# Kernel tuning notes

Hardware: AMD Instinct MI355X
Metric: run time of the kernel (lower is better)

Reference implementation:

```python
import jax, jax.numpy as jnp
import numpy as np

B, D, T, R = 8, 128, 32768, 2
C = D // R  # reduced channel dim = 64


def conv1x1(x, w, b):
    # x: [B, Cin, T], w: [Cout, Cin], b: [Cout] -> [B, Cout, T]
    return jnp.einsum('oi,bit->bot', w, x) + b[None, :, None]


def setup_inputs() -> dict:
    key = jax.random.key(0)
    ks = jax.random.split(key, 16)
    inp = {
        'x1': jax.random.normal(ks[0], (B, D, T), dtype=jnp.float32),
        'x2': jnp.zeros((B, D, T), dtype=jnp.float32),  # unused in encoder stage
        'mask': jnp.ones((B, 1, T), dtype=jnp.float32),
        # 1x1 conv projections (weights squeezed to [out, in])
        'wq': jax.random.normal(ks[1], (C, D), dtype=jnp.float32) * 0.05,
        'bq': jnp.zeros((C,), dtype=jnp.float32),
        'wk': jax.random.normal(ks[2], (C, D), dtype=jnp.float32) * 0.05,
        'bk': jnp.zeros((C,), dtype=jnp.float32),
        'wv': jax.random.normal(ks[3], (C, D), dtype=jnp.float32) * 0.05,
        'bv': jnp.zeros((C,), dtype=jnp.float32),
        # E, F: Linear(C -> C) with bias
        'we': jax.random.normal(ks[4], (C, C), dtype=jnp.float32) * 0.1,
        'be': jnp.zeros((C,), dtype=jnp.float32),
        'wf': jax.random.normal(ks[5], (C, C), dtype=jnp.float32) * 0.1,
        'bf': jnp.zeros((C,), dtype=jnp.float32),
        # output 1x1 conv: C -> D
        'wo': jax.random.normal(ks[6], (D, C), dtype=jnp.float32) * 0.05,
        'bo': jnp.zeros((D,), dtype=jnp.float32),
    }
    return inp


def reference(x1, x2, mask, wq, bq, wk, bk, wv, bv, we, be, wf, bf, wo, bo):
    # Q/K/V projections (encoder stage: value from x1; x2 unused)
    Q = conv1x1(x1, wq, bq)              # [B, C, T]
    K = conv1x1(x1, wk, bk)              # [B, C, T]
    V = conv1x1(x1, wv, bv)              # [B, C, T]
    # K = E(K^T): [B, T, C] @ we^T + be
    Kp = jnp.einsum('bct,oc->bto', K, we) + be  # [B, T, C]
    # S = Q @ Kp -> [B, C, C], scaled by sqrt(last dim)
    S = jnp.einsum('bct,btk->bck', Q, Kp)
    P = jax.nn.softmax(S / jnp.sqrt(jnp.asarray(S.shape[-1], S.dtype)), axis=-1)
    # dropout is identity in eval mode
    # V = (F(V^T))^T: [B, C, T]
    Vp = jnp.einsum('bct,oc->bot', V, wf) + bf[None, :, None]  # [B, C, T]
    out = jnp.einsum('bck,bkt->bct', P, Vp)  # [B, C, T]
    out = conv1x1(jax.nn.relu(out), wo, bo)  # [B, D, T]
    return out * mask[:, 0:1, :]
```

## Files before the change

### kernel.cpp

```cpp
#include <hip/hip_runtime.h>
#include <stdint.h>
#include <stddef.h>

#define B_ 8
#define D_ 128
#define T_ 32768
#define C_ 64
#define NCH_ 64

typedef __bf16 bf16;
typedef __bf16 bf16x4 __attribute__((ext_vector_type(4)));
typedef __bf16 bf16x8 __attribute__((ext_vector_type(8)));
typedef float f32x2 __attribute__((ext_vector_type(2)));
typedef float f32x4 __attribute__((ext_vector_type(4)));
typedef float f32x16 __attribute__((ext_vector_type(16)));

__device__ __forceinline__ f32x16 zero16() {
  f32x16 z;
#pragma unroll
  for (int i = 0; i < 16; ++i) z[i] = 0.f;
  return z;
}

__global__ __launch_bounds__(256) void k0_zero(float* __restrict__ p, int n)
{
  int i = blockIdx.x * 256 + threadIdx.x;
  if (i < n) p[i] = 0.f;
}

__global__ __launch_bounds__(256, 2) void k1_gram(
    const float* __restrict__ x1,
    const float* __restrict__ we, const float* __restrict__ wk,
    const float* __restrict__ bk, const float* __restrict__ be,
    const float* __restrict__ wf, const float* __restrict__ wv,
    const float* __restrict__ bv, const float* __restrict__ bfv,
    const float* __restrict__ wo,
    float* __restrict__ G, float* __restrict__ r,
    float* __restrict__ wkp, float* __restrict__ wvp,
    float* __restrict__ bkp, float* __restrict__ bvp,
    bf16* __restrict__ wobf,
    float* __restrict__ gpart)
{
  const int blk = blockIdx.x;
  const int tid = threadIdx.x;
  const int ngram = B_ * NCH_;

  if (blk >= ngram) {
    const int wb = blk - ngram;
    if (wb < 64) {
      const float* wa  = (wb < 32) ? we : wf;
      const float* wb2 = (wb < 32) ? wk : wv;
      float* outw      = (wb < 32) ? wkp : wvp;
      const int idx = (wb & 31) * 256 + tid;
      const int o = idx >> 7, d = idx & 127;
      float s = 0.f;
      for (int c = 0; c < 64; ++c) s += wa[o * 64 + c] * wb2[c * 128 + d];
      outw[idx] = s;
      if (tid < 64) {
        if (wb == 0) {
          float t = 0.f;
          for (int c = 0; c < 64; ++c) t += we[tid * 64 + c] * bk[c];
          bkp[tid] = t + be[tid];
        } else if (wb == 32) {
          float t = 0.f;
          for (int c = 0; c < 64; ++c) t += wf[tid * 64 + c] * bv[c];
          bvp[tid] = t + bfv[tid];
        }
      }
    } else {
      const int idx = (wb - 64) * 256 + tid;
      wobf[idx] = (bf16)wo[idx];
    }
    return;
  }

  __shared__ bf16 x_s[128 * 264];

  const int b  = blk / NCH_;
  const int ch = blk & (NCH_ - 1);
  const int t0 = ch * (T_ / NCH_);
  const int wave = tid >> 6, lane = tid & 63;
  const int lrow = lane & 31, lk = lane >> 5;
  const int qa = wave >> 1, qb = wave & 1;

  const float* xb = x1 + (size_t)b * D_ * T_ + t0;

  f32x16 acc00 = zero16(), acc01 = zero16(), acc10 = zero16(), acc11 = zero16();
  float rsum = 0.f;

  const bf16* A0  = &x_s[(64 * qa + lrow) * 264 + 8 * lk];
  const bf16* A1  = A0 + 32 * 264;
  const bf16* Bb0 = &x_s[(64 * qb + lrow) * 264 + 8 * lk];
  const bf16* Bb1 = Bb0 + 32 * 264;

  for (int s = 0; s < 2; ++s) {
    const float* xs = xb + s * 256;
    if (s) __syncthreads();
#pragma unroll
    for (int g = 0; g < 4; ++g) {
      f32x4 pre[8];
#pragma unroll
      for (int i = 0; i < 8; ++i) {
        const int row = 32 * wave + 8 * g + i;
        pre[i] = *(const f32x4*)(xs + (size_t)row * T_ + 4 * lane);
      }
#pragma unroll
      for (int i = 0; i < 8; ++i) {
        const int row = 32 * wave + 8 * g + i;
        bf16x4 h;
#pragma unroll
        for (int j = 0; j < 4; ++j) h[j] = (bf16)pre[i][j];
        *(bf16x4*)&x_s[row * 264 + 4 * lane] = h;
      }
    }
    __syncthreads();
#pragma unroll
    for (int k = 0; k < 16; ++k) {
      bf16x8 fa0 = *(const bf16x8*)(A0 + 16 * k);
      bf16x8 fa1 = *(const bf16x8*)(A1 + 16 * k);
      bf16x8 fb0 = *(const bf16x8*)(Bb0 + 16 * k);
      bf16x8 fb1 = *(const bf16x8*)(Bb1 + 16 * k);
      bf16x8 own = qb ? fa1 : fa0;
#pragma unroll
      for (int j = 0; j < 8; ++j) rsum += (float)own[j];
      acc00 = __builtin_amdgcn_mfma_f32_32x32x16_bf16(fa0, fb0, acc00, 0, 0, 0);
      acc01 = __builtin_amdgcn_mfma_f32_32x32x16_bf16(fa0, fb1, acc01, 0, 0, 0);
      acc10 = __builtin_amdgcn_mfma_f32_32x32x16_bf16(fa1, fb0, acc10, 0, 0, 0);
      acc11 = __builtin_amdgcn_mfma_f32_32x32x16_bf16(fa1, fb1, acc11, 0, 0, 0);
    }
  }

  if (gpart) {
    float* gp = gpart + (size_t)blk * 16384 + wave * 4096;
#pragma unroll
    for (int rr = 0; rr < 16; ++rr) {
      f32x4 v;
      v[0] = acc00[rr]; v[1] = acc01[rr]; v[2] = acc10[rr]; v[3] = acc11[rr];
      *(f32x4*)(gp + rr * 256 + lane * 4) = v;
    }
  } else {
    float* gb = G + (size_t)b * 16384;
#pragma unroll
    for (int rr = 0; rr < 16; ++rr) {
      const int rloc = (rr & 3) + 8 * (rr >> 2) + 4 * lk;
      const int r0 = 64 * qa + rloc, r1 = 64 * qa + 32 + rloc;
      const int c0 = 64 * qb + lrow, c1 = 64 * qb + 32 + lrow;
      atomicAdd(&gb[r0 * 128 + c0], acc00[rr]);
      atomicAdd(&gb[r0 * 128 + c1], acc01[rr]);
      atomicAdd(&gb[r1 * 128 + c0], acc10[rr]);
      atomicAdd(&gb[r1 * 128 + c1], acc11[rr]);
    }
  }
  float rtot = rsum + __shfl_xor(rsum, 32, 64);
  if (lk == 0) atomicAdd(&r[b * 128 + 32 * wave + lrow], rtot);
}

__global__ __launch_bounds__(256) void k2_reduce(
    const float* __restrict__ gpart, float* __restrict__ G)
{
  const int g4 = blockIdx.x * 256 + threadIdx.x;
  const int b = g4 >> 12;
  const int e4 = g4 & 4095;
  const f32x4* p = (const f32x4*)(gpart + ((size_t)b * NCH_) * 16384) + e4;
  f32x4 s = {0.f, 0.f, 0.f, 0.f};
#pragma unroll 8
  for (int ch = 0; ch < NCH_; ++ch) s += p[(size_t)ch * 4096];

  const int w = e4 >> 10, rr = (e4 >> 6) & 15, lane = e4 & 63;
  const int lk = lane >> 5, lrow = lane & 31;
  const int qa = w >> 1, qb = w & 1;
  const int rloc = (rr & 3) + 8 * (rr >> 2) + 4 * lk;
  const int r0 = 64 * qa + rloc, c0 = 64 * qb + lrow;
  float* Gb = G + (size_t)b * 16384;
  Gb[r0 * 128 + c0]               = s[0];
  Gb[r0 * 128 + c0 + 32]          = s[1];
  Gb[(r0 + 32) * 128 + c0]        = s[2];
  Gb[(r0 + 32) * 128 + c0 + 32]   = s[3];
}

__global__ __launch_bounds__(128) void k3_softmax(
    const float* __restrict__ wq, const float* __restrict__ bq,
    const float* __restrict__ G, const float* __restrict__ r,
    const float* __restrict__ wkp, const float* __restrict__ wvp,
    const float* __restrict__ bkp, const float* __restrict__ bvp,
    bf16* __restrict__ attw, float* __restrict__ attb)
{
  const int b = blockIdx.x >> 6, c = blockIdx.x & 63;
  const int tid = threadIdx.x;
  __shared__ float sM[128], sR[128], sQ[128], sP[64];
  __shared__ float sRed;

  const float* Gb = G + (size_t)b * 16384;
  const float* wqc = wq + c * 128;

  const float rv = r[b * 128 + tid];
  sR[tid] = rv;
  float m = 0.f;
  for (int j = 0; j < 128; ++j) m += wqc[j] * Gb[j * 128 + tid];
  sM[tid] = m;
  sQ[tid] = wqc[tid] * rv;
  __syncthreads();

  if (tid < 64) {
    float q2 = sQ[tid] + sQ[tid + 64];
#pragma unroll
    for (int off = 32; off; off >>= 1) q2 += __shfl_xor(q2, off, 64);
    if (tid == 0) sRed = q2;
  }
  __syncthreads();
  const float qr = sRed;
  const float bqc = bq[c];

  if (tid < 64) {
    const int k = tid;
    float s = 0.f, wkr = 0.f;
    for (int i = 0; i < 128; ++i) {
      const float w = wkp[k * 128 + i];
      s += sM[i] * w;
      wkr += sR[i] * w;
    }
    const float bk2 = bkp[k];
    float logit = (s + bqc * wkr + bk2 * qr + (float)T_ * bqc * bk2) * 0.125f;
    float mx = logit;
#pragma unroll
    for (int off = 32; off; off >>= 1) mx = fmaxf(mx, __shfl_xor(mx, off, 64));
    const float e = __expf(logit - mx);
    float sum = e;
#pragma unroll
    for (int off = 32; off; off >>= 1) sum += __shfl_xor(sum, off, 64);
    sP[k] = e / sum;
  }
  __syncthreads();

  {
    float aw = 0.f;
    for (int k = 0; k < 64; ++k) aw += sP[k] * wvp[k * 128 + tid];
    attw[((size_t)b * 64 + c) * 128 + tid] = (bf16)aw;
  }
  if (tid < 64) {
    float pb = sP[tid] * bvp[tid];
#pragma unroll
    for (int off = 32; off; off >>= 1) pb += __shfl_xor(pb, off, 64);
    if (tid == 0) attb[b * 64 + c] = pb;
  }
}

__global__ __launch_bounds__(256, 4) void k4_out(
    const float* __restrict__ x1, const float* __restrict__ mask,
    const bf16* __restrict__ wobf, const float* __restrict__ bo,
    const bf16* __restrict__ attw, const float* __restrict__ attb,
    float* __restrict__ out)
{
  __shared__ __attribute__((aligned(16))) char ubuf[64 * 132 * 4];
  bf16*  m1  = (bf16*)ubuf;
  float* o_s = (float*)ubuf;
  __shared__ float bo_s[128];
  __shared__ float ab_s[64];

  const int b = blockIdx.x >> 8;
  const int t0 = (blockIdx.x & 255) << 7;
  const int tid = threadIdx.x;
  const int wave = tid >> 6, lane = tid & 63;
  const int lrow = lane & 31, lk = lane >> 5;
  const int tcol = 32 * wave + lrow;

  if (tid < 128) bo_s[tid] = bo[tid];
  if (tid < 64) ab_s[tid] = attb[b * 64 + tid];
  __syncthreads();

  const float* xc = x1 + (size_t)b * D_ * T_ + t0 + tcol;
  const bf16* awb = attw + (size_t)b * 8192;

  f32x16 p0 = zero16(), p1 = zero16();
#pragma unroll
  for (int k0 = 0; k0 < 8; ++k0) {
    bf16x8 a0 = *(const bf16x8*)(awb + (size_t)lrow * 128 + 16 * k0 + 8 * lk);
    bf16x8 a1 = *(const bf16x8*)(awb + (size_t)(32 + lrow) * 128 + 16 * k0 + 8 * lk);
    bf16x8 bx;
#pragma unroll
    for (int j = 0; j < 8; ++j)
      bx[j] = (bf16)xc[(size_t)(16 * k0 + 8 * lk + j) * T_];
    p0 = __builtin_amdgcn_mfma_f32_32x32x16_bf16(a0, bx, p0, 0, 0, 0);
    p1 = __builtin_amdgcn_mfma_f32_32x32x16_bf16(a1, bx, p1, 0, 0, 0);
  }
  bf16* mrow = &m1[tcol * 72];
#pragma unroll
  for (int rr = 0; rr < 16; ++rr) {
    const int row = (rr & 3) + 8 * (rr >> 2) + 4 * lk;
    mrow[row]      = (bf16)fmaxf(p0[rr] + ab_s[row], 0.f);
    mrow[32 + row] = (bf16)fmaxf(p1[rr] + ab_s[32 + row], 0.f);
  }

  f32x16 q0 = zero16(), q1 = zero16(), q2 = zero16(), q3 = zero16();
#pragma unroll
  for (int k0 = 0; k0 < 4; ++k0) {
    bf16x8 bm = *(const bf16x8*)(mrow + 16 * k0 + 8 * lk);
    bf16x8 w0 = *(const bf16x8*)(wobf + (size_t)(lrow) * 64 + 16 * k0 + 8 * lk);
    bf16x8 w1 = *(const bf16x8*)(wobf + (size_t)(32 + lrow) * 64 + 16 * k0 + 8 * lk);
    bf16x8 w2 = *(const bf16x8*)(wobf + (size_t)(64 + lrow) * 64 + 16 * k0 + 8 * lk);
    bf16x8 w3 = *(const bf16x8*)(wobf + (size_t)(96 + lrow) * 64 + 16 * k0 + 8 * lk);
    q0 = __builtin_amdgcn_mfma_f32_32x32x16_bf16(w0, bm, q0, 0, 0, 0);
    q1 = __builtin_amdgcn_mfma_f32_32x32x16_bf16(w1, bm, q1, 0, 0, 0);
    q2 = __builtin_amdgcn_mfma_f32_32x32x16_bf16(w2, bm, q2, 0, 0, 0);
    q3 = __builtin_amdgcn_mfma_f32_32x32x16_bf16(w3, bm, q3, 0, 0, 0);
  }

  const float mv = mask[(size_t)b * T_ + t0 + tcol];
  float* ob = out + (size_t)b * D_ * T_ + t0;

  __syncthreads();
#pragma unroll
  for (int rr = 0; rr < 16; ++rr) {
    const int rloc = (rr & 3) + 8 * (rr >> 2) + 4 * lk;
    o_s[rloc * 132 + tcol]        = (q0[rr] + bo_s[rloc]) * mv;
    o_s[(32 + rloc) * 132 + tcol] = (q1[rr] + bo_s[32 + rloc]) * mv;
  }
  __syncthreads();
#pragma unroll
  for (int i = 0; i < 16; ++i) {
    const int dl = 16 * wave + i;
    f32x2 v = *(const f32x2*)(o_s + dl * 132 + 2 * lane);
    *(f32x2*)(ob + (size_t)dl * T_ + 2 * lane) = v;
  }
  __syncthreads();
#pragma unroll
  for (int rr = 0; rr < 16; ++rr) {
    const int rloc = (rr & 3) + 8 * (rr >> 2) + 4 * lk;
    o_s[rloc * 132 + tcol]        = (q2[rr] + bo_s[64 + rloc]) * mv;
    o_s[(32 + rloc) * 132 + tcol] = (q3[rr] + bo_s[96 + rloc]) * mv;
  }
  __syncthreads();
#pragma unroll
  for (int i = 0; i < 16; ++i) {
    const int dl = 16 * wave + i;
    f32x2 v = *(const f32x2*)(o_s + dl * 132 + 2 * lane);
    *(f32x2*)(ob + (size_t)(64 + dl) * T_ + 2 * lane) = v;
  }
}

extern "C" void kernel_launch(void* const* d_in, const int* in_sizes, int n_in,
                              void* d_out, int out_size, void* d_ws, size_t ws_size,
                              hipStream_t stream)
{
  const float* x1   = (const float*)d_in[0];
  const float* mask = (const float*)d_in[2];
  const float* wq   = (const float*)d_in[3];
  const float* bq   = (const float*)d_in[4];
  const float* wk   = (const float*)d_in[5];
  const float* bk   = (const float*)d_in[6];
  const float* wv   = (const float*)d_in[7];
  const float* bv   = (const float*)d_in[8];
  const float* we   = (const float*)d_in[9];
  const float* be   = (const float*)d_in[10];
  const float* wf   = (const float*)d_in[11];
  const float* bfv  = (const float*)d_in[12];
  const float* wo   = (const float*)d_in[13];
  const float* bo   = (const float*)d_in[14];
  float* out = (float*)d_out;

  char* base = (char*)d_ws;
  size_t off = 0;
  float* G    = (float*)(base + off); off += (size_t)B_ * 16384 * 4;
  float* r    = (float*)(base + off); off += (size_t)B_ * 128 * 4;
  float* wkp  = (float*)(base + off); off += 8192 * 4;
  float* wvp  = (float*)(base + off); off += 8192 * 4;
  float* bkp  = (float*)(base + off); off += 64 * 4;
  float* bvp  = (float*)(base + off); off += 64 * 4;
  float* attb = (float*)(base + off); off += (size_t)B_ * 64 * 4;
  bf16* attw  = (bf16*)(base + off);  off += (size_t)B_ * 64 * 128 * 2;
  bf16* wobf  = (bf16*)(base + off);  off += 8192 * 2;
  off = (off + 15) & ~(size_t)15;
  float* gpart = (float*)(base + off);
  const size_t need = off + (size_t)B_ * NCH_ * 16384 * 4;
  const bool use_part = (ws_size >= need);
  if (!use_part) gpart = nullptr;

  if (use_part) {
    k0_zero<<<(B_ * 128 + 255) / 256, 256, 0, stream>>>(r, B_ * 128);
  } else {
    const int nzero = B_ * 16384 + B_ * 128;
    k0_zero<<<(nzero + 255) / 256, 256, 0, stream>>>(G, nzero);
  }
  k1_gram<<<B_ * NCH_ + 96, 256, 0, stream>>>(
      x1, we, wk, bk, be, wf, wv, bv, bfv, wo,
      G, r, wkp, wvp, bkp, bvp, wobf, gpart);
  if (use_part)
    k2_reduce<<<(B_ * 16384) / (256 * 4), 256, 0, stream>>>(gpart, G);
  k3_softmax<<<B_ * 64, 128, 0, stream>>>(wq, bq, G, r, wkp, wvp, bkp, bvp, attw, attb);
  k4_out<<<B_ * (T_ / 128), 256, 0, stream>>>(x1, mask, wobf, bo, attw, attb, out);
}
```

Measured before the change: 375.7 us.

## Stage x1 tile through LDS in output kernel and reduce row sums without atomics

The output kernel now loads x1 as contiguous float2 rows per wave, converts them to bf16 and stages them in shared memory in two halves before the MFMA reads, replacing strided per-lane scalar global loads. Row-sum partials from the gram kernel are written to a per-chunk buffer and summed in the reduce kernel, which removes the zero-fill launch and the atomics. The change adds shared memory use and an extra barrier per half, which may reduce occupancy in the output kernel, and it needs more workspace for the row-sum partials.

```diff
diff --git a/kernel.cpp b/kernel.cpp
--- a/kernel.cpp
+++ b/kernel.cpp
@@ -9,6 +9,7 @@
 #define NCH_ 64
 
 typedef __bf16 bf16;
+typedef __bf16 bf16x2 __attribute__((ext_vector_type(2)));
 typedef __bf16 bf16x4 __attribute__((ext_vector_type(4)));
 typedef __bf16 bf16x8 __attribute__((ext_vector_type(8)));
 typedef float f32x2 __attribute__((ext_vector_type(2)));
@@ -39,7 +40,7 @@
     float* __restrict__ wkp, float* __restrict__ wvp,
     float* __restrict__ bkp, float* __restrict__ bvp,
     bf16* __restrict__ wobf,
-    float* __restrict__ gpart)
+    float* __restrict__ gpart, float* __restrict__ rpart)
 {
   const int blk = blockIdx.x;
   const int tid = threadIdx.x;
@@ -130,6 +131,8 @@
     }
   }
 
+  float rtot = rsum + __shfl_xor(rsum, 32, 64);
+
   if (gpart) {
     float* gp = gpart + (size_t)blk * 16384 + wave * 4096;
 #pragma unroll
@@ -138,6 +141,7 @@
       v[0] = acc00[rr]; v[1] = acc01[rr]; v[2] = acc10[rr]; v[3] = acc11[rr];
       *(f32x4*)(gp + rr * 256 + lane * 4) = v;
     }
+    if (lk == 0) rpart[(size_t)blk * 128 + 32 * wave + lrow] = rtot;
   } else {
     float* gb = G + (size_t)b * 16384;
 #pragma unroll
@@ -150,32 +154,41 @@
       atomicAdd(&gb[r1 * 128 + c0], acc10[rr]);
       atomicAdd(&gb[r1 * 128 + c1], acc11[rr]);
     }
-  }
-  float rtot = rsum + __shfl_xor(rsum, 32, 64);
-  if (lk == 0) atomicAdd(&r[b * 128 + 32 * wave + lrow], rtot);
+    if (lk == 0) atomicAdd(&r[b * 128 + 32 * wave + lrow], rtot);
+  }
 }
 
 __global__ __launch_bounds__(256) void k2_reduce(
-    const float* __restrict__ gpart, float* __restrict__ G)
+    const float* __restrict__ gpart, const float* __restrict__ rpart,
+    float* __restrict__ G, float* __restrict__ r)
 {
   const int g4 = blockIdx.x * 256 + threadIdx.x;
-  const int b = g4 >> 12;
-  const int e4 = g4 & 4095;
-  const f32x4* p = (const f32x4*)(gpart + ((size_t)b * NCH_) * 16384) + e4;
-  f32x4 s = {0.f, 0.f, 0.f, 0.f};
+  if (g4 < 32768) {
+    const int b = g4 >> 12;
+    const int e4 = g4 & 4095;
+    const f32x4* p = (const f32x4*)(gpart + ((size_t)b * NCH_) * 16384) + e4;
+    f32x4 s = {0.f, 0.f, 0.f, 0.f};
 #pragma unroll 8
-  for (int ch = 0; ch < NCH_; ++ch) s += p[(size_t)ch * 4096];
-
-  const int w = e4 >> 10, rr = (e4 >> 6) & 15, lane = e4 & 63;
-  const int lk = lane >> 5, lrow = lane & 31;
-  const int qa = w >> 1, qb = w & 1;
-  const int rloc = (rr & 3) + 8 * (rr >> 2) + 4 * lk;
-  const int r0 = 64 * qa + rloc, c0 = 64 * qb + lrow;
-  float* Gb = G + (size_t)b * 16384;
-  Gb[r0 * 128 + c0]               = s[0];
-  Gb[r0 * 128 + c0 + 32]          = s[1];
-  Gb[(r0 + 32) * 128 + c0]        = s[2];
-  Gb[(r0 + 32) * 128 + c0 + 32]   = s[3];
+    for (int ch = 0; ch < NCH_; ++ch) s += p[(size_t)ch * 4096];
+
+    const int w = e4 >> 10, rr = (e4 >> 6) & 15, lane = e4 & 63;
+    const int lk = lane >> 5, lrow = lane & 31;
+    const int qa = w >> 1, qb = w & 1;
+    const int rloc = (rr & 3) + 8 * (rr >> 2) + 4 * lk;
+    const int r0 = 64 * qa + rloc, c0 = 64 * qb + lrow;
+    float* Gb = G + (size_t)b * 16384;
+    Gb[r0 * 128 + c0]               = s[0];
+    Gb[r0 * 128 + c0 + 32]          = s[1];
+    Gb[(r0 + 32) * 128 + c0]        = s[2];
+    Gb[(r0 + 32) * 128 + c0 + 32]   = s[3];
+  } else {
+    const int idx = g4 - 32768;
+    const int b = idx >> 7, d = idx & 127;
+    float s = 0.f;
+    for (int ch = 0; ch < NCH_; ++ch)
+      s += rpart[((size_t)(b * NCH_ + ch)) * 128 + d];
+    r[b * 128 + d] = s;
+  }
 }
 
 __global__ __launch_bounds__(128) void k3_softmax(
@@ -251,9 +264,10 @@
     const bf16* __restrict__ attw, const float* __restrict__ attb,
     float* __restrict__ out)
 {
-  __shared__ __attribute__((aligned(16))) char ubuf[64 * 132 * 4];
-  bf16*  m1  = (bf16*)ubuf;
-  float* o_s = (float*)ubuf;
+  __shared__ __attribute__((aligned(16))) char ubuf[35328];
+  bf16*  x_lin = (bf16*)ubuf;
+  bf16*  m1    = (bf16*)(ubuf + 16896);
+  float* o_s   = (float*)ubuf;
   __shared__ float bo_s[128];
   __shared__ float ab_s[64];
 
@@ -266,23 +280,41 @@
 
   if (tid < 128) bo_s[tid] = bo[tid];
   if (tid < 64) ab_s[tid] = attb[b * 64 + tid];
-  __syncthreads();
-
-  const float* xc = x1 + (size_t)b * D_ * T_ + t0 + tcol;
+
+  const float* xb = x1 + (size_t)b * D_ * T_ + t0;
   const bf16* awb = attw + (size_t)b * 8192;
 
   f32x16 p0 = zero16(), p1 = zero16();
-#pragma unroll
-  for (int k0 = 0; k0 < 8; ++k0) {
-    bf16x8 a0 = *(const bf16x8*)(awb + (size_t)lrow * 128 + 16 * k0 + 8 * lk);
-    bf16x8 a1 = *(const bf16x8*)(awb + (size_t)(32 + lrow) * 128 + 16 * k0 + 8 * lk);
-    bf16x8 bx;
-#pragma unroll
-    for (int j = 0; j < 8; ++j)
-      bx[j] = (bf16)xc[(size_t)(16 * k0 + 8 * lk + j) * T_];
-    p0 = __builtin_amdgcn_mfma_f32_32x32x16_bf16(a0, bx, p0, 0, 0, 0);
-    p1 = __builtin_amdgcn_mfma_f32_32x32x16_bf16(a1, bx, p1, 0, 0, 0);
-  }
+
+#pragma unroll
+  for (int dh = 0; dh < 2; ++dh) {
+    if (dh) __syncthreads();
+    const float* xs = xb + (size_t)(64 * dh + 16 * wave) * T_;
+    f32x2 pr[16];
+#pragma unroll
+    for (int i = 0; i < 16; ++i)
+      pr[i] = *(const f32x2*)(xs + (size_t)i * T_ + 2 * lane);
+#pragma unroll
+    for (int i = 0; i < 16; ++i) {
+      bf16x2 h; h[0] = (bf16)pr[i][0]; h[1] = (bf16)pr[i][1];
+      *(bf16x2*)&x_lin[(16 * wave + i) * 132 + 2 * lane] = h;
+    }
+    __syncthreads();
+
+#pragma unroll
+    for (int k0 = 0; k0 < 4; ++k0) {
+      const int kg = 4 * dh + k0;
+      bf16x8 a0 = *(const bf16x8*)(awb + (size_t)lrow * 128 + 16 * kg + 8 * lk);
+      bf16x8 a1 = *(const bf16x8*)(awb + (size_t)(32 + lrow) * 128 + 16 * kg + 8 * lk);
+      bf16x8 bx;
+#pragma unroll
+      for (int j = 0; j < 8; ++j)
+        bx[j] = x_lin[(16 * k0 + 8 * lk + j) * 132 + tcol];
+      p0 = __builtin_amdgcn_mfma_f32_32x32x16_bf16(a0, bx, p0, 0, 0, 0);
+      p1 = __builtin_amdgcn_mfma_f32_32x32x16_bf16(a1, bx, p1, 0, 0, 0);
+    }
+  }
+
   bf16* mrow = &m1[tcol * 72];
 #pragma unroll
   for (int rr = 0; rr < 16; ++rr) {
@@ -370,22 +402,20 @@
   bf16* attw  = (bf16*)(base + off);  off += (size_t)B_ * 64 * 128 * 2;
   bf16* wobf  = (bf16*)(base + off);  off += 8192 * 2;
   off = (off + 15) & ~(size_t)15;
-  float* gpart = (float*)(base + off);
-  const size_t need = off + (size_t)B_ * NCH_ * 16384 * 4;
-  const bool use_part = (ws_size >= need);
-  if (!use_part) gpart = nullptr;
-
-  if (use_part) {
-    k0_zero<<<(B_ * 128 + 255) / 256, 256, 0, stream>>>(r, B_ * 128);
-  } else {
+  float* gpart = (float*)(base + off); off += (size_t)B_ * NCH_ * 16384 * 4;
+  float* rpart = (float*)(base + off); off += (size_t)B_ * NCH_ * 128 * 4;
+  const bool use_part = (ws_size >= off);
+  if (!use_part) { gpart = nullptr; rpart = nullptr; }
+
+  if (!use_part) {
     const int nzero = B_ * 16384 + B_ * 128;
     k0_zero<<<(nzero + 255) / 256, 256, 0, stream>>>(G, nzero);
   }
   k1_gram<<<B_ * NCH_ + 96, 256, 0, stream>>>(
       x1, we, wk, bk, be, wf, wv, bv, bfv, wo,
-      G, r, wkp, wvp, bkp, bvp, wobf, gpart);
+      G, r, wkp, wvp, bkp, bvp, wobf, gpart, rpart);
   if (use_part)
-    k2_reduce<<<(B_ * 16384) / (256 * 4), 256, 0, stream>>>(gpart, G);
+    k2_reduce<<<132, 256, 0, stream>>>(gpart, rpart, G, r);
   k3_softmax<<<B_ * 64, 128, 0, stream>>>(wq, bq, G, r, wkp, wvp, bkp, bvp, attw, attb);
   k4_out<<<B_ * (T_ / 128), 256, 0, stream>>>(x1, mask, wobf, bo, attw, attb, out);
 }
```

Result: no change. 370.9 us (-1.3%).
